# Kernel tuning notes

Measured on AMD Instinct MI355X. Metric: run time of the kernel, lower is better.

## Reference

```python
import jax, jax.numpy as jnp
import numpy as np


def _binarize_kernel_wise(w):
    # Bi-ViT LinearBi (Qmodes.kernel_wise): per-output-channel scale alpha = mean(|w|)
    # quantized weight w_q = alpha * sign(w).  w: [out, in]
    alpha = jnp.mean(jnp.abs(w), axis=1, keepdims=True)  # [out, 1]
    return alpha * jnp.sign(w)


def setup_inputs() -> dict:
    key = jax.random.key(0)
    k_x, k_w1, k_b1, k_w2, k_b2 = jax.random.split(key, 5)
    B, N, C, H = 64, 197, 768, 3072
    x = jax.random.normal(k_x, (B, N, C), dtype=jnp.float32)
    w1 = jax.random.normal(k_w1, (H, C), dtype=jnp.float32) * 0.02
    b1 = jax.random.normal(k_b1, (H,), dtype=jnp.float32) * 0.02
    w2 = jax.random.normal(k_w2, (C, H), dtype=jnp.float32) * 0.02
    b2 = jax.random.normal(k_b2, (C,), dtype=jnp.float32) * 0.02
    return {"x": x, "w1": w1, "b1": b1, "w2": w2, "b2": b2}


def reference(x, w1, b1, w2, b2):
    # fc1 (binarized linear, kernel-wise scales)
    w1_q = _binarize_kernel_wise(w1)
    h = jnp.einsum('bnc,hc->bnh', x, w1_q) + b1
    # GELU (exact, erf-based as torch nn.GELU default) then clip to [-10, 10]
    h = jnp.clip(jax.nn.gelu(h, approximate=False), -10.0, 10.0)
    # dropout p=0.0 -> identity
    w2_q = _binarize_kernel_wise(w2)
    out = jnp.einsum('bnh,ch->bnc', h, w2_q) + b2
    return out
```

## Files before the change

### kernel.cpp

```cpp
#include <hip/hip_runtime.h>
#include <hip/hip_bf16.h>
#include <cstdint>
#include <cstddef>


typedef __bf16 bf16x8 __attribute__((ext_vector_type(8)));
typedef __bf16 bf16x4 __attribute__((ext_vector_type(4)));
typedef float floatx16 __attribute__((ext_vector_type(16)));

__device__ __forceinline__ void async_load16(const void* g, void* l) {
    __builtin_amdgcn_global_load_lds(
        (const __attribute__((address_space(1))) void*)g,
        (__attribute__((address_space(3))) void*)l,
        16, 0, 0);
}

__global__ __launch_bounds__(256) void x_to_bf16(
    const float* __restrict__ in, __hip_bfloat16* __restrict__ out, int n4)
{
    int i = blockIdx.x * 256 + threadIdx.x;
    if (i < n4) {
        float4 v = ((const float4*)in)[i];
        bf16x4 o;
        o[0] = (__bf16)v.x; o[1] = (__bf16)v.y;
        o[2] = (__bf16)v.z; o[3] = (__bf16)v.w;
        ((bf16x4*)out)[i] = o;
    }
}

__global__ __launch_bounds__(256) void bin_prep(
    const float* __restrict__ w,
    __hip_bfloat16* __restrict__ sgn,
    float* __restrict__ alpha,
    int cols4)
{
    const int row = blockIdx.x;
    const float4* wr = (const float4*)w + (size_t)row * cols4;
    bf16x4* sr = (bf16x4*)sgn + (size_t)row * cols4;
    float s = 0.0f;
    for (int c = threadIdx.x; c < cols4; c += 256) {
        float4 v = wr[c];
        s += fabsf(v.x) + fabsf(v.y) + fabsf(v.z) + fabsf(v.w);
        bf16x4 o;
        o[0] = (__bf16)(v.x > 0.0f ? 1.0f : (v.x < 0.0f ? -1.0f : 0.0f));
        o[1] = (__bf16)(v.y > 0.0f ? 1.0f : (v.y < 0.0f ? -1.0f : 0.0f));
        o[2] = (__bf16)(v.z > 0.0f ? 1.0f : (v.z < 0.0f ? -1.0f : 0.0f));
        o[3] = (__bf16)(v.w > 0.0f ? 1.0f : (v.w < 0.0f ? -1.0f : 0.0f));
        sr[c] = o;
    }
    #pragma unroll
    for (int off = 32; off > 0; off >>= 1) s += __shfl_down(s, off, 64);
    __shared__ float wsum[4];
    const int lane = threadIdx.x & 63;
    const int wv = threadIdx.x >> 6;
    if (lane == 0) wsum[wv] = s;
    __syncthreads();
    if (threadIdx.x == 0) {
        float t = wsum[0] + wsum[1] + wsum[2] + wsum[3];
        alpha[row] = t / (float)(cols4 * 4);
    }
}

__device__ __forceinline__ void store_val(__hip_bfloat16* C, size_t idx, float v) {
    C[idx] = __float2bfloat16(v);
}
__device__ __forceinline__ void store_val(float* C, size_t idx, float v) {
    C[idx] = v;
}

template <int TM, bool DO_GELU, typename OutT>
__global__ __launch_bounds__(256) void gemm_bin(
    const __hip_bfloat16* __restrict__ A,
    const __hip_bfloat16* __restrict__ S,
    const float* __restrict__ alpha,
    const float* __restrict__ bias,
    OutT* __restrict__ C,
    int M, int N, int K)
{
    constexpr int TN = 128;
    constexpr int TK = 64;
    constexpr int ASEG = TM / 8;
    constexpr int RSEG = ASEG + TN / 8;
    constexpr int PW   = RSEG / 4;
    constexpr int WMT  = TM / 2;
    constexpr int MI   = WMT / 32;

    __shared__ __align__(16) __hip_bfloat16 sA[TM * TK];
    __shared__ __align__(16) __hip_bfloat16 sB[TN * TK];

    const int tid = threadIdx.x;
    const int wave = tid >> 6;
    const int lane = tid & 63;
    const int bm = blockIdx.y * TM;
    const int bn = blockIdx.x * TN;

    const int wm = (wave & 1) * WMT;
    const int wn = (wave >> 1) * 64;
    const int ln = lane & 31;
    const int kh = lane >> 5;
    const int e3 = lane & 7;

    const int crow = lane >> 3;
    const int ccol = ((lane & 7) ^ crow) * 8;

    floatx16 acc[MI][2];
    #pragma unroll
    for (int i = 0; i < MI; i++)
        #pragma unroll
        for (int j = 0; j < 2; j++)
            #pragma unroll
            for (int r = 0; r < 16; r++)
                acc[i][j][r] = 0.0f;

    for (int k0 = 0; k0 < K; k0 += TK) {
        #pragma unroll
        for (int t = 0; t < PW; t++) {
            const int seg = wave * PW + t;
            if (seg < ASEG) {
                const int r = seg * 8 + crow;
                int ar = bm + r;
                ar = ar < M ? ar : (M - 1);
                async_load16(A + (size_t)ar * K + (k0 + ccol), (void*)(sA + seg * 512));
            } else {
                const int r = (seg - ASEG) * 8 + crow;
                async_load16(S + (size_t)(bn + r) * K + (k0 + ccol),
                             (void*)(sB + (seg - ASEG) * 512));
            }
        }
        __syncthreads();

        #pragma unroll
        for (int ks = 0; ks < 4; ks++) {
            const int slot = ((ks * 2 + kh) ^ e3) * 8;
            bf16x8 af[MI], bfv[2];
            #pragma unroll
            for (int i = 0; i < MI; i++)
                af[i] = *(const bf16x8*)(sA + (wm + i * 32 + ln) * TK + slot);
            #pragma unroll
            for (int j = 0; j < 2; j++)
                bfv[j] = *(const bf16x8*)(sB + (wn + j * 32 + ln) * TK + slot);
            #pragma unroll
            for (int i = 0; i < MI; i++)
                #pragma unroll
                for (int j = 0; j < 2; j++)
                    acc[i][j] = __builtin_amdgcn_mfma_f32_32x32x16_bf16(
                        af[i], bfv[j], acc[i][j], 0, 0, 0);
        }
        __syncthreads();
    }

    float al[2], bi[2];
    #pragma unroll
    for (int j = 0; j < 2; j++) {
        const int col = bn + wn + j * 32 + ln;
        al[j] = alpha[col];
        bi[j] = bias[col];
    }
    #pragma unroll
    for (int i = 0; i < MI; i++) {
        #pragma unroll
        for (int r = 0; r < 16; r++) {
            const int row = bm + wm + i * 32 + (r & 3) + 8 * (r >> 2) + 4 * kh;
            if (row < M) {
                #pragma unroll
                for (int j = 0; j < 2; j++) {
                    float v = acc[i][j][r] * al[j] + bi[j];
                    if (DO_GELU) {
                        v = 0.5f * v * (1.0f + erff(v * 0.70710678118654752f));
                        v = fminf(fmaxf(v, -10.0f), 10.0f);
                    }
                    store_val(C, (size_t)row * N + (bn + wn + j * 32 + ln), v);
                }
            }
        }
    }
}

extern "C" void kernel_launch(void* const* d_in, const int* in_sizes, int n_in,
                              void* d_out, int out_size, void* d_ws, size_t ws_size,
                              hipStream_t stream) {
    const float* x  = (const float*)d_in[0];
    const float* w1 = (const float*)d_in[1];
    const float* b1 = (const float*)d_in[2];
    const float* w2 = (const float*)d_in[3];
    const float* b2 = (const float*)d_in[4];

    const int M = 64 * 197;
    const int Cd = 768;
    const int Hd = 3072;

    char* ws = (char*)d_ws;
    __hip_bfloat16* xb   = (__hip_bfloat16*)ws;
    __hip_bfloat16* sgn1 = xb + (size_t)M * Cd;
    __hip_bfloat16* sgn2 = sgn1 + (size_t)Hd * Cd;
    float* alpha1 = (float*)(sgn2 + (size_t)Cd * Hd);
    float* alpha2 = alpha1 + Hd;
    __hip_bfloat16* hbuf = (__hip_bfloat16*)(alpha2 + Cd);

    const int n4 = (M * Cd) / 4;
    x_to_bf16<<<(n4 + 255) / 256, 256, 0, stream>>>(x, xb, n4);
    bin_prep<<<Hd, 256, 0, stream>>>(w1, sgn1, alpha1, Cd / 4);
    bin_prep<<<Cd, 256, 0, stream>>>(w2, sgn2, alpha2, Hd / 4);

    gemm_bin<128, true, __hip_bfloat16>
        <<<dim3(Hd / 128, (M + 127) / 128), 256, 0, stream>>>(
        xb, sgn1, alpha1, b1, hbuf, M, Hd, Cd);
    gemm_bin<64, false, float>
        <<<dim3(Cd / 128, M / 64), 256, 0, stream>>>(
        hbuf, sgn2, alpha2, b2, (float*)d_out, M, Cd, Hd);
}
```

Measured before the change: 295.9 us.

## Switch GEMMs to 16x16x32 MFMA and merge prep kernels into one launch

Both GEMM kernels now use the 16x16x32 bf16 MFMA instead of 32x32x16. Each wave computes a grid of 16x16 tiles with a new LDS fragment indexing and XOR swizzle, and the epilogue writes four contiguous rows per lane group. Separately, the x-to-bf16 conversion and the two weight-binarization kernels are merged into one launch that dispatches on block index, removing two kernel launches. The per-wave tile shape is unchanged, but the smaller MFMA issues more instructions and fragment loads per K step, and the merged prep kernel hardcodes the row widths 192 and 768.

```diff
diff --git a/kernel.cpp b/kernel.cpp
--- a/kernel.cpp
+++ b/kernel.cpp
@@ -6,7 +6,7 @@
 
 typedef __bf16 bf16x8 __attribute__((ext_vector_type(8)));
 typedef __bf16 bf16x4 __attribute__((ext_vector_type(4)));
-typedef float floatx16 __attribute__((ext_vector_type(16)));
+typedef float floatx4 __attribute__((ext_vector_type(4)));
 
 __device__ __forceinline__ void async_load16(const void* g, void* l) {
     __builtin_amdgcn_global_load_lds(
@@ -15,26 +15,31 @@
         16, 0, 0);
 }
 
-__global__ __launch_bounds__(256) void x_to_bf16(
-    const float* __restrict__ in, __hip_bfloat16* __restrict__ out, int n4)
+__global__ __launch_bounds__(256) void prep_all(
+    const float* __restrict__ x,
+    const float* __restrict__ w1,
+    const float* __restrict__ w2,
+    __hip_bfloat16* __restrict__ xb,
+    __hip_bfloat16* __restrict__ sgn1, float* __restrict__ alpha1,
+    __hip_bfloat16* __restrict__ sgn2, float* __restrict__ alpha2,
+    int ncvt)
 {
-    int i = blockIdx.x * 256 + threadIdx.x;
-    if (i < n4) {
-        float4 v = ((const float4*)in)[i];
+    const int b = blockIdx.x;
+    if (b < ncvt) {
+        const int i = b * 256 + threadIdx.x;
+        float4 v = ((const float4*)x)[i];
         bf16x4 o;
         o[0] = (__bf16)v.x; o[1] = (__bf16)v.y;
         o[2] = (__bf16)v.z; o[3] = (__bf16)v.w;
-        ((bf16x4*)out)[i] = o;
-    }
-}
-
-__global__ __launch_bounds__(256) void bin_prep(
-    const float* __restrict__ w,
-    __hip_bfloat16* __restrict__ sgn,
-    float* __restrict__ alpha,
-    int cols4)
-{
-    const int row = blockIdx.x;
+        ((bf16x4*)xb)[i] = o;
+        return;
+    }
+    const float* w; __hip_bfloat16* sgn; float* alpha; int cols4; int row;
+    if (b < ncvt + 3072) {
+        w = w1; sgn = sgn1; alpha = alpha1; cols4 = 192; row = b - ncvt;
+    } else {
+        w = w2; sgn = sgn2; alpha = alpha2; cols4 = 768; row = b - ncvt - 3072;
+    }
     const float4* wr = (const float4*)w + (size_t)row * cols4;
     bf16x4* sr = (bf16x4*)sgn + (size_t)row * cols4;
     float s = 0.0f;
@@ -79,11 +84,11 @@
 {
     constexpr int TN = 128;
     constexpr int TK = 64;
+    constexpr int WMT = TM / 2;
+    constexpr int MI  = WMT / 16;
     constexpr int ASEG = TM / 8;
     constexpr int RSEG = ASEG + TN / 8;
     constexpr int PW   = RSEG / 4;
-    constexpr int WMT  = TM / 2;
-    constexpr int MI   = WMT / 32;
 
     __shared__ __align__(16) __hip_bfloat16 sA[TM * TK];
     __shared__ __align__(16) __hip_bfloat16 sB[TN * TK];
@@ -96,20 +101,20 @@
 
     const int wm = (wave & 1) * WMT;
     const int wn = (wave >> 1) * 64;
-    const int ln = lane & 31;
-    const int kh = lane >> 5;
-    const int e3 = lane & 7;
+    const int lr = lane & 15;
+    const int kq = lane >> 4;
+    const int e3 = lr & 7;
 
     const int crow = lane >> 3;
     const int ccol = ((lane & 7) ^ crow) * 8;
 
-    floatx16 acc[MI][2];
+    floatx4 acc[MI][4];
     #pragma unroll
     for (int i = 0; i < MI; i++)
         #pragma unroll
-        for (int j = 0; j < 2; j++)
-            #pragma unroll
-            for (int r = 0; r < 16; r++)
+        for (int j = 0; j < 4; j++)
+            #pragma unroll
+            for (int r = 0; r < 4; r++)
                 acc[i][j][r] = 0.0f;
 
     for (int k0 = 0; k0 < K; k0 += TK) {
@@ -130,46 +135,47 @@
         __syncthreads();
 
         #pragma unroll
-        for (int ks = 0; ks < 4; ks++) {
-            const int slot = ((ks * 2 + kh) ^ e3) * 8;
-            bf16x8 af[MI], bfv[2];
+        for (int ks = 0; ks < 2; ks++) {
+            const int slot = ((ks << 2) | kq) ^ e3;
+            bf16x8 af[MI], bfv[4];
             #pragma unroll
             for (int i = 0; i < MI; i++)
-                af[i] = *(const bf16x8*)(sA + (wm + i * 32 + ln) * TK + slot);
-            #pragma unroll
-            for (int j = 0; j < 2; j++)
-                bfv[j] = *(const bf16x8*)(sB + (wn + j * 32 + ln) * TK + slot);
+                af[i] = *(const bf16x8*)(sA + (wm + i * 16 + lr) * TK + slot * 8);
+            #pragma unroll
+            for (int j = 0; j < 4; j++)
+                bfv[j] = *(const bf16x8*)(sB + (wn + j * 16 + lr) * TK + slot * 8);
             #pragma unroll
             for (int i = 0; i < MI; i++)
                 #pragma unroll
-                for (int j = 0; j < 2; j++)
-                    acc[i][j] = __builtin_amdgcn_mfma_f32_32x32x16_bf16(
+                for (int j = 0; j < 4; j++)
+                    acc[i][j] = __builtin_amdgcn_mfma_f32_16x16x32_bf16(
                         af[i], bfv[j], acc[i][j], 0, 0, 0);
         }
         __syncthreads();
     }
 
-    float al[2], bi[2];
-    #pragma unroll
-    for (int j = 0; j < 2; j++) {
-        const int col = bn + wn + j * 32 + ln;
+    float al[4], bi[4];
+    #pragma unroll
+    for (int j = 0; j < 4; j++) {
+        const int col = bn + wn + j * 16 + lr;
         al[j] = alpha[col];
         bi[j] = bias[col];
     }
     #pragma unroll
     for (int i = 0; i < MI; i++) {
-        #pragma unroll
-        for (int r = 0; r < 16; r++) {
-            const int row = bm + wm + i * 32 + (r & 3) + 8 * (r >> 2) + 4 * kh;
+        const int row0 = bm + wm + i * 16 + kq * 4;
+        #pragma unroll
+        for (int r = 0; r < 4; r++) {
+            const int row = row0 + r;
             if (row < M) {
                 #pragma unroll
-                for (int j = 0; j < 2; j++) {
+                for (int j = 0; j < 4; j++) {
                     float v = acc[i][j][r] * al[j] + bi[j];
                     if (DO_GELU) {
                         v = 0.5f * v * (1.0f + erff(v * 0.70710678118654752f));
                         v = fminf(fmaxf(v, -10.0f), 10.0f);
                     }
-                    store_val(C, (size_t)row * N + (bn + wn + j * 32 + ln), v);
+                    store_val(C, (size_t)row * N + (bn + wn + j * 16 + lr), v);
                 }
             }
         }
@@ -197,10 +203,9 @@
     float* alpha2 = alpha1 + Hd;
     __hip_bfloat16* hbuf = (__hip_bfloat16*)(alpha2 + Cd);
 
-    const int n4 = (M * Cd) / 4;
-    x_to_bf16<<<(n4 + 255) / 256, 256, 0, stream>>>(x, xb, n4);
-    bin_prep<<<Hd, 256, 0, stream>>>(w1, sgn1, alpha1, Cd / 4);
-    bin_prep<<<Cd, 256, 0, stream>>>(w2, sgn2, alpha2, Hd / 4);
+    const int ncvt = (M * Cd) / 4 / 256;
+    prep_all<<<ncvt + Hd + Cd, 256, 0, stream>>>(
+        x, w1, w2, xb, sgn1, alpha1, sgn2, alpha2, ncvt);
 
     gemm_bin<128, true, __hip_bfloat16>
         <<<dim3(Hd / 128, (M + 127) / 128), 256, 0, stream>>>(
```

Result: no change. 293.1 us (-1.0%).
